# Optimization experiments

Hardware: AMD Instinct MI355X
Metric: run time of the kernel (lower is better)

## Reference

```python
import jax, jax.numpy as jnp
import numpy as np

DIM = 1024
HEADS = 16


def setup_inputs() -> dict:
    key = jax.random.key(0)
    ks = jax.random.split(key, 5)
    x = jax.random.normal(ks[0], (2, 2048, DIM), dtype=jnp.float32)
    # nn.Linear init-like scaling
    qkv_w = jax.random.normal(ks[1], (3 * DIM, DIM), dtype=jnp.float32) * (1.0 / np.sqrt(DIM))
    qkv_b = jax.random.normal(ks[2], (3 * DIM,), dtype=jnp.float32) * 0.02
    proj_w = jax.random.normal(ks[3], (DIM, DIM), dtype=jnp.float32) * (1.0 / np.sqrt(DIM))
    proj_b = jax.random.normal(ks[4], (DIM,), dtype=jnp.float32) * 0.02
    return {"x": x, "qkv_w": qkv_w, "qkv_b": qkv_b, "proj_w": proj_w, "proj_b": proj_b}


def reference(x, qkv_w, qkv_b, proj_w, proj_b):
    B, N, C = x.shape
    H = HEADS
    Dh = C // H
    scale = Dh ** -0.5
    # qkv: [B, N, 3C] -> [3, B, H, N, Dh]
    qkv = (x @ qkv_w.T + qkv_b).reshape(B, N, 3, H, Dh).transpose(2, 0, 3, 1, 4)
    q, k, v = qkv[0], qkv[1], qkv[2]
    attn = jnp.einsum('bhnd,bhmd->bhnm', q, k) * scale
    attn = jax.nn.softmax(attn, axis=-1)
    out = jnp.einsum('bhnm,bhmd->bhnd', attn, v)  # [B, H, N, Dh]
    out = out.transpose(0, 2, 1, 3).reshape(B, N, C)
    return out @ proj_w.T + proj_b
```

## Files before the change

kernel.cpp:

```cpp
#include <hip/hip_runtime.h>
#include <stdint.h>

#define DIM    1024
#define NHEADS 16
#define DH     64
#define SEQ    2048
#define BATCH  2
#define BHEADS (BATCH * NHEADS)
#define MROWS  (BATCH * SEQ)
#define SL2E   0.18033688011112042f

typedef __attribute__((ext_vector_type(8))) short bf16x8;
typedef __attribute__((ext_vector_type(4))) float f32x4;
typedef unsigned short ushort_t;

#define GLDS(gp, lp) __builtin_amdgcn_global_load_lds( \
    (__attribute__((address_space(1))) void*)(gp), \
    (__attribute__((address_space(3))) void*)(lp), 16, 0, 0)

__device__ inline ushort_t f2bf(float f) {
    unsigned u = __builtin_bit_cast(unsigned, f);
    u += 0x7FFFu + ((u >> 16) & 1u);
    return (ushort_t)(u >> 16);
}

__global__ __launch_bounds__(256) void cvt_kernel(
    const float* __restrict__ s0, const float* __restrict__ s1, const float* __restrict__ s2,
    ushort_t* __restrict__ d0, ushort_t* __restrict__ d1, ushort_t* __restrict__ d2)
{
    const int N0 = MROWS * DIM;
    const int N1 = 3 * DIM * DIM;
    const int N2 = DIM * DIM;
    int e = (blockIdx.x * 256 + threadIdx.x) << 2;
    const float* src; ushort_t* dst;
    if (e < N0)                { src = s0 + e;             dst = d0 + e; }
    else if (e < N0 + N1)      { src = s1 + (e - N0);      dst = d1 + (e - N0); }
    else if (e < N0 + N1 + N2) { src = s2 + (e - N0 - N1); dst = d2 + (e - N0 - N1); }
    else return;
    float4 f = *(const float4*)src;
    ushort4 o;
    o.x = f2bf(f.x); o.y = f2bf(f.y); o.z = f2bf(f.z); o.w = f2bf(f.w);
    *(ushort4*)dst = o;
}

__global__ __launch_bounds__(256) void qkv_gemm(
    const ushort_t* __restrict__ A, const ushort_t* __restrict__ W,
    const float* __restrict__ bias,
    ushort_t* __restrict__ Qw, ushort_t* __restrict__ Kw, ushort_t* __restrict__ Vt)
{
    __shared__ ushort_t smem[128 * 136];
    ushort_t* As = smem;
    ushort_t* Bs = smem + 128 * 64;

    const int tid  = threadIdx.x;
    const int lane = tid & 63;
    const int wave = tid >> 6;
    const int quad = lane >> 4;
    const int l16  = lane & 15;
    const int wm   = (wave >> 1) * 64;
    const int wn   = (wave & 1) * 64;
    const int bm   = blockIdx.x * 128;
    const int bn   = blockIdx.y * 128;
    const int Rl   = lane >> 3;
    const int pp   = lane & 7;

    f32x4 acc[4][4];
    for (int i = 0; i < 4; i++)
        for (int j = 0; j < 4; j++)
            for (int r = 0; r < 4; r++) acc[i][j][r] = 0.f;

    for (int kk = 0; kk < DIM; kk += 64) {
        __syncthreads();
        for (int j = 0; j < 4; j++) {
            int Rb = j * 32 + wave * 8;
            int R  = Rb + Rl;
            int c  = pp ^ (R & 7);
            GLDS(A + (size_t)(bm + R) * DIM + kk + c * 8, As + Rb * 64 + lane * 8);
            GLDS(W + (size_t)(bn + R) * DIM + kk + c * 8, Bs + Rb * 64 + lane * 8);
        }
        __syncthreads();

        for (int kh = 0; kh < 2; kh++) {
            bf16x8 a[4], b[4];
            for (int mi = 0; mi < 4; mi++) {
                int r = wm + mi * 16 + l16;
                a[mi] = *(const bf16x8*)(As + r * 64 + (((kh * 4 + quad) ^ (r & 7)) << 3));
            }
            for (int ni = 0; ni < 4; ni++) {
                int r = wn + ni * 16 + l16;
                b[ni] = *(const bf16x8*)(Bs + r * 64 + (((kh * 4 + quad) ^ (r & 7)) << 3));
            }
            for (int mi = 0; mi < 4; mi++)
                for (int ni = 0; ni < 4; ni++)
                    acc[mi][ni] = __builtin_amdgcn_mfma_f32_16x16x32_bf16(a[mi], b[ni], acc[mi][ni], 0, 0, 0);
        }
    }

    __syncthreads();
    const int three = bn >> 10;
    const float scale = (three == 0) ? SL2E : 1.0f;
    for (int ni = 0; ni < 4; ni++) {
        int cl   = wn + ni * 16 + l16;
        float bv = bias[bn + cl];
        for (int mi = 0; mi < 4; mi++)
            for (int reg = 0; reg < 4; reg++) {
                int r = wm + mi * 16 + quad * 4 + reg;
                smem[r * 136 + cl] = f2bf((acc[mi][ni][reg] + bv) * scale);
            }
    }
    __syncthreads();

    const int b = bm >> 11, npos0 = bm & 2047;
    if (three < 2) {
        int r = tid >> 1, hh = tid & 1;
        int hc = (bn + hh * 64) & 1023;
        int h  = hc >> 6;
        ushort_t* dst = (three == 0 ? Qw : Kw) + ((size_t)(b * NHEADS + h) * SEQ + npos0 + r) * DH;
        const ushort_t* srcp = smem + r * 136 + hh * 64;
        for (int s = 0; s < 8; s++)
            *(uint4*)(dst + s * 8) = *(const uint4*)(srcp + s * 8);
    } else {
        int c = tid & 127, hh = tid >> 7;
        int hc = (bn + c) & 1023;
        int h  = hc >> 6, d = hc & 63;
        ushort_t* dst = Vt + ((size_t)(b * NHEADS + h) * DH + d) * SEQ + npos0 + hh * 64;
        for (int s = 0; s < 8; s++) {
            union { ushort_t u[8]; uint4 v; } tmp;
            for (int k2 = 0; k2 < 8; k2++)
                tmp.u[k2] = smem[(hh * 64 + s * 8 + k2) * 136 + c];
            *(uint4*)(dst + s * 8) = tmp.v;
        }
    }
}

struct AttnSmem {
    ushort_t KV[2][2][2][32 * 64];
    ushort_t QP[128 * 64];
};
union AttnSmemU {
    AttnSmem m;
    float Lb[128][66];
};

__global__ __launch_bounds__(512, 4) void attn_kernel(
    const ushort_t* __restrict__ Qw, const ushort_t* __restrict__ Kw,
    const ushort_t* __restrict__ Vt, ushort_t* __restrict__ Ao)
{
    __shared__ AttnSmemU sh;

    const int tid  = threadIdx.x;
    const int lane = tid & 63;
    const int wave = tid >> 6;
    const int grp  = wave >> 2;
    const int wg   = wave & 3;
    const int quad = lane >> 4;
    const int l16  = lane & 15;
    const int bh   = blockIdx.y;
    const int q0   = blockIdx.x * 128;
    const int Rl   = lane >> 3;
    const int pp   = lane & 7;

    const ushort_t* Qh = Qw + (size_t)bh * SEQ * DH;
    const ushort_t* Kh = Kw + (size_t)bh * SEQ * DH;
    const ushort_t* Vh = Vt + (size_t)bh * DH * SEQ;

    for (int j = 0; j < 2; j++) {
        int Rb = j * 64 + wave * 8;
        int R  = Rb + Rl;
        int c  = pp ^ (R & 7);
        GLDS(Qh + (size_t)(q0 + R) * DH + c * 8, sh.m.QP + Rb * 64 + lane * 8);
    }
    {
        int t  = grp;
        int Rk = wg * 8 + Rl;
        int ck = pp ^ (Rk & 7);
        GLDS(Kh + (size_t)(t * 32 + Rk) * DH + ck * 8, sh.m.KV[0][grp][0] + wg * 512 + lane * 8);
        int Rv = wg * 16 + (lane >> 2);
        int pv = lane & 3;
        int cv = pv ^ ((Rv >> 1) & 3);
        GLDS(Vh + (size_t)Rv * SEQ + t * 32 + cv * 8, sh.m.KV[0][grp][1] + wg * 512 + lane * 8);
    }
    __syncthreads();

    bf16x8 qf[2][2];
    for (int mi = 0; mi < 2; mi++)
        for (int kh = 0; kh < 2; kh++) {
            int r = wg * 32 + mi * 16 + l16;
            qf[mi][kh] = *(const bf16x8*)(sh.m.QP + r * 64 + (((kh * 4 + quad) ^ (r & 7)) << 3));
        }
    __syncthreads();

    bf16x8 vones;
    for (int i = 0; i < 8; i++) vones[i] = (short)0x3F80;

    f32x4 oacc[2][4], liacc[2];
    for (int mi = 0; mi < 2; mi++) {
        for (int r = 0; r < 4; r++) liacc[mi][r] = 0.f;
        for (int d = 0; d < 4; d++)
            for (int r = 0; r < 4; r++) oacc[mi][d][r] = 0.f;
    }

    ushort_t* Pw = sh.m.QP + wave * 1024;

    const int NIT = 32;
    for (int it = 0; it < NIT; it++) {
        const int phase = it & 1;
        if (it < NIT - 1) {
            int np = phase ^ 1;
            int t  = 2 * (it + 1) + grp;
            int Rk = wg * 8 + Rl;
            int ck = pp ^ (Rk & 7);
            GLDS(Kh + (size_t)(t * 32 + Rk) * DH + ck * 8, sh.m.KV[np][grp][0] + wg * 512 + lane * 8);
            int Rv = wg * 16 + (lane >> 2);
            int pv = lane & 3;
            int cv = pv ^ ((Rv >> 1) & 3);
            GLDS(Vh + (size_t)Rv * SEQ + t * 32 + cv * 8, sh.m.KV[np][grp][1] + wg * 512 + lane * 8);
        }
        const ushort_t* Ksb = sh.m.KV[phase][grp][0];
        const ushort_t* Vsb = sh.m.KV[phase][grp][1];

        f32x4 s[2][2];
        for (int mi = 0; mi < 2; mi++)
            for (int nf = 0; nf < 2; nf++)
                for (int r = 0; r < 4; r++) s[mi][nf][r] = 0.f;
        for (int kh = 0; kh < 2; kh++)
            for (int nf = 0; nf < 2; nf++) {
                int r = nf * 16 + l16;
                bf16x8 kf = *(const bf16x8*)(Ksb + r * 64 + (((kh * 4 + quad) ^ (r & 7)) << 3));
                s[0][nf] = __builtin_amdgcn_mfma_f32_16x16x32_bf16(kf, qf[0][kh], s[0][nf], 0, 0, 0);
                s[1][nf] = __builtin_amdgcn_mfma_f32_16x16x32_bf16(kf, qf[1][kh], s[1][nf], 0, 0, 0);
            }

        for (int mi = 0; mi < 2; mi++) {
            int row = mi * 16 + l16;
            int swz = (row >> 1) & 3;
            for (int nf = 0; nf < 2; nf++) {
                unsigned u0 = __builtin_bit_cast(unsigned, __builtin_amdgcn_exp2f(s[mi][nf][0])) + 0x8000u;
                unsigned u1 = __builtin_bit_cast(unsigned, __builtin_amdgcn_exp2f(s[mi][nf][1])) + 0x8000u;
                unsigned u2 = __builtin_bit_cast(unsigned, __builtin_amdgcn_exp2f(s[mi][nf][2])) + 0x8000u;
                unsigned u3 = __builtin_bit_cast(unsigned, __builtin_amdgcn_exp2f(s[mi][nf][3])) + 0x8000u;
                uint2 pk;
                pk.x = __builtin_amdgcn_perm(u1, u0, 0x07060302u);
                pk.y = __builtin_amdgcn_perm(u3, u2, 0x07060302u);
                int jp = (nf * 2 + (quad >> 1)) ^ swz;
                *(uint2*)(Pw + row * 32 + jp * 8 + (quad & 1) * 4) = pk;
            }
        }

        bf16x8 pf[2];
        for (int mi = 0; mi < 2; mi++) {
            int row = mi * 16 + l16;
            int jp  = quad ^ ((row >> 1) & 3);
            pf[mi] = *(const bf16x8*)(Pw + row * 32 + jp * 8);
        }

        liacc[0] = __builtin_amdgcn_mfma_f32_16x16x32_bf16(pf[0], vones, liacc[0], 0, 0, 0);
        liacc[1] = __builtin_amdgcn_mfma_f32_16x16x32_bf16(pf[1], vones, liacc[1], 0, 0, 0);

        for (int df = 0; df < 4; df++) {
            int r  = df * 16 + l16;
            int jp = quad ^ ((r >> 1) & 3);
            bf16x8 vf = *(const bf16x8*)(Vsb + r * 32 + jp * 8);
            oacc[0][df] = __builtin_amdgcn_mfma_f32_16x16x32_bf16(pf[0], vf, oacc[0][df], 0, 0, 0);
            oacc[1][df] = __builtin_amdgcn_mfma_f32_16x16x32_bf16(pf[1], vf, oacc[1][df], 0, 0, 0);
        }

        __syncthreads();
    }

    const int b = bh >> 4, h = bh & 15;
    if (grp == 1) {
        for (int mi = 0; mi < 2; mi++)
            for (int reg = 0; reg < 4; reg++) {
                int row = wg * 32 + mi * 16 + quad * 4 + reg;
                for (int df = 0; df < 4; df++)
                    sh.Lb[row][df * 16 + l16] = oacc[mi][df][reg];
                if (l16 == 0) sh.Lb[row][64] = liacc[mi][reg];
            }
    }
    __syncthreads();
    if (grp == 0) {
        for (int mi = 0; mi < 2; mi++)
            for (int reg = 0; reg < 4; reg++) {
                int row   = wg * 32 + mi * 16 + quad * 4 + reg;
                float inv = 1.0f / (liacc[mi][reg] + sh.Lb[row][64]);
                int grow  = q0 + row;
                for (int df = 0; df < 4; df++) {
                    int col = df * 16 + l16;
                    float o = oacc[mi][df][reg] + sh.Lb[row][col];
                    Ao[((size_t)b * SEQ + grow) * DIM + h * 64 + col] = f2bf(o * inv);
                }
            }
    }
}

__global__ __launch_bounds__(256, 4) void proj_gemm(
    const ushort_t* __restrict__ A, const ushort_t* __restrict__ W,
    const float* __restrict__ bias, float* __restrict__ Cout)
{
    __shared__ ushort_t As[128 * 64];
    __shared__ ushort_t Bs[64 * 64];

    const int tid  = threadIdx.x;
    const int lane = tid & 63;
    const int wave = tid >> 6;
    const int quad = lane >> 4;
    const int l16  = lane & 15;
    const int wm   = (wave >> 1) * 64;
    const int wn   = (wave & 1) * 32;
    const int bm   = blockIdx.x * 128;
    const int bn   = blockIdx.y * 64;
    const int Rl   = lane >> 3;
    const int pp   = lane & 7;

    f32x4 acc[4][2];
    for (int i = 0; i < 4; i++)
        for (int j = 0; j < 2; j++)
            for (int r = 0; r < 4; r++) acc[i][j][r] = 0.f;

    for (int kk = 0; kk < DIM; kk += 64) {
        __syncthreads();
        for (int j = 0; j < 4; j++) {
            int Rb = j * 32 + wave * 8;
            int R  = Rb + Rl;
            int c  = pp ^ (R & 7);
            GLDS(A + (size_t)(bm + R) * DIM + kk + c * 8, As + Rb * 64 + lane * 8);
        }
        for (int j = 0; j < 2; j++) {
            int Rb = j * 32 + wave * 8;
            int R  = Rb + Rl;
            int c  = pp ^ (R & 7);
            GLDS(W + (size_t)(bn + R) * DIM + kk + c * 8, Bs + Rb * 64 + lane * 8);
        }
        __syncthreads();

        for (int kh = 0; kh < 2; kh++) {
            bf16x8 a[4], b[2];
            for (int mi = 0; mi < 4; mi++) {
                int r = wm + mi * 16 + l16;
                a[mi] = *(const bf16x8*)(As + r * 64 + (((kh * 4 + quad) ^ (r & 7)) << 3));
            }
            for (int ni = 0; ni < 2; ni++) {
                int r = wn + ni * 16 + l16;
                b[ni] = *(const bf16x8*)(Bs + r * 64 + (((kh * 4 + quad) ^ (r & 7)) << 3));
            }
            for (int mi = 0; mi < 4; mi++)
                for (int ni = 0; ni < 2; ni++)
                    acc[mi][ni] = __builtin_amdgcn_mfma_f32_16x16x32_bf16(a[mi], b[ni], acc[mi][ni], 0, 0, 0);
        }
    }

    for (int mi = 0; mi < 4; mi++) {
        for (int ni = 0; ni < 2; ni++) {
            int col  = bn + wn + ni * 16 + l16;
            float bv = bias[col];
            for (int reg = 0; reg < 4; reg++) {
                int row = bm + wm + mi * 16 + quad * 4 + reg;
                Cout[(size_t)row * DIM + col] = acc[mi][ni][reg] + bv;
            }
        }
    }
}

extern "C" void kernel_launch(void* const* d_in, const int* in_sizes, int n_in,
                              void* d_out, int out_size, void* d_ws, size_t ws_size,
                              hipStream_t stream) {
    const float* x      = (const float*)d_in[0];
    const float* qkv_w  = (const float*)d_in[1];
    const float* qkv_b  = (const float*)d_in[2];
    const float* proj_w = (const float*)d_in[3];
    const float* proj_b = (const float*)d_in[4];
    float* out = (float*)d_out;

    ushort_t* xb      = (ushort_t*)d_ws;
    ushort_t* qkv_wb  = xb      + (size_t)MROWS * DIM;
    ushort_t* proj_wb = qkv_wb  + (size_t)3 * DIM * DIM;
    ushort_t* Qw      = proj_wb + (size_t)DIM * DIM;
    ushort_t* Kw      = Qw      + (size_t)BHEADS * SEQ * DH;
    ushort_t* Vt      = Kw      + (size_t)BHEADS * SEQ * DH;
    ushort_t* Ao      = Vt      + (size_t)BHEADS * SEQ * DH;

    const int total_cvt = MROWS * DIM + 3 * DIM * DIM + DIM * DIM;
    cvt_kernel<<<total_cvt / (4 * 256), 256, 0, stream>>>(x, qkv_w, proj_w, xb, qkv_wb, proj_wb);
    qkv_gemm<<<dim3(MROWS / 128, (3 * DIM) / 128), 256, 0, stream>>>(xb, qkv_wb, qkv_b, Qw, Kw, Vt);
    attn_kernel<<<dim3(SEQ / 128, BHEADS), 512, 0, stream>>>(Qw, Kw, Vt, Ao);
    proj_gemm<<<dim3(MROWS / 128, DIM / 64), 256, 0, stream>>>(Ao, proj_wb, proj_b, out);
}
```

Baseline: 190.5 us.

## Double-buffer LDS tiles in QKV and projection GEMMs to overlap loads

Both GEMM kernels now keep two LDS stages and issue the global-to-LDS loads for the next K tile before computing on the current one. Explicit vmcnt waits and raw barriers replace the two __syncthreads per iteration. The goal is to hide global memory latency behind MFMA work. In exchange, shared memory use per block roughly doubles, which can lower occupancy, and the hand-counted vmcnt values must match the number of loads in flight.

```diff
diff --git a/kernel.cpp b/kernel.cpp
--- a/kernel.cpp
+++ b/kernel.cpp
@@ -48,9 +48,10 @@
     const float* __restrict__ bias,
     ushort_t* __restrict__ Qw, ushort_t* __restrict__ Kw, ushort_t* __restrict__ Vt)
 {
-    __shared__ ushort_t smem[128 * 136];
-    ushort_t* As = smem;
-    ushort_t* Bs = smem + 128 * 64;
+    __shared__ union {
+        ushort_t stage[2][2][128 * 64];
+        ushort_t T[128 * 136];
+    } sm;
 
     const int tid  = threadIdx.x;
     const int lane = tid & 63;
@@ -69,34 +70,53 @@
         for (int j = 0; j < 4; j++)
             for (int r = 0; r < 4; r++) acc[i][j][r] = 0.f;
 
-    for (int kk = 0; kk < DIM; kk += 64) {
-        __syncthreads();
-        for (int j = 0; j < 4; j++) {
-            int Rb = j * 32 + wave * 8;
-            int R  = Rb + Rl;
-            int c  = pp ^ (R & 7);
-            GLDS(A + (size_t)(bm + R) * DIM + kk + c * 8, As + Rb * 64 + lane * 8);
-            GLDS(W + (size_t)(bn + R) * DIM + kk + c * 8, Bs + Rb * 64 + lane * 8);
-        }
-        __syncthreads();
-
+    for (int j = 0; j < 4; j++) {
+        int Rb = j * 32 + wave * 8;
+        int R  = Rb + Rl;
+        int c  = pp ^ (R & 7);
+        GLDS(A + (size_t)(bm + R) * DIM + c * 8, sm.stage[0][0] + Rb * 64 + lane * 8);
+        GLDS(W + (size_t)(bn + R) * DIM + c * 8, sm.stage[0][1] + Rb * 64 + lane * 8);
+    }
+
+    const int NT = DIM / 64;
+    for (int t = 0; t < NT; t++) {
+        if (t < NT - 1) {
+            int kk = (t + 1) * 64;
+            ushort_t* As1 = sm.stage[(t + 1) & 1][0];
+            ushort_t* Bs1 = sm.stage[(t + 1) & 1][1];
+            for (int j = 0; j < 4; j++) {
+                int Rb = j * 32 + wave * 8;
+                int R  = Rb + Rl;
+                int c  = pp ^ (R & 7);
+                GLDS(A + (size_t)(bm + R) * DIM + kk + c * 8, As1 + Rb * 64 + lane * 8);
+                GLDS(W + (size_t)(bn + R) * DIM + kk + c * 8, Bs1 + Rb * 64 + lane * 8);
+            }
+            __asm volatile("s_waitcnt vmcnt(8)" ::: "memory");
+        } else {
+            __asm volatile("s_waitcnt vmcnt(0)" ::: "memory");
+        }
+        __asm volatile("s_barrier" ::: "memory");
+
+        const ushort_t* Asb = sm.stage[t & 1][0];
+        const ushort_t* Bsb = sm.stage[t & 1][1];
         for (int kh = 0; kh < 2; kh++) {
             bf16x8 a[4], b[4];
             for (int mi = 0; mi < 4; mi++) {
                 int r = wm + mi * 16 + l16;
-                a[mi] = *(const bf16x8*)(As + r * 64 + (((kh * 4 + quad) ^ (r & 7)) << 3));
+                a[mi] = *(const bf16x8*)(Asb + r * 64 + (((kh * 4 + quad) ^ (r & 7)) << 3));
             }
             for (int ni = 0; ni < 4; ni++) {
                 int r = wn + ni * 16 + l16;
-                b[ni] = *(const bf16x8*)(Bs + r * 64 + (((kh * 4 + quad) ^ (r & 7)) << 3));
+                b[ni] = *(const bf16x8*)(Bsb + r * 64 + (((kh * 4 + quad) ^ (r & 7)) << 3));
             }
             for (int mi = 0; mi < 4; mi++)
                 for (int ni = 0; ni < 4; ni++)
                     acc[mi][ni] = __builtin_amdgcn_mfma_f32_16x16x32_bf16(a[mi], b[ni], acc[mi][ni], 0, 0, 0);
         }
-    }
-
-    __syncthreads();
+        __asm volatile("s_waitcnt lgkmcnt(0)" ::: "memory");
+        __asm volatile("s_barrier" ::: "memory");
+    }
+
     const int three = bn >> 10;
     const float scale = (three == 0) ? SL2E : 1.0f;
     for (int ni = 0; ni < 4; ni++) {
@@ -105,7 +125,7 @@
         for (int mi = 0; mi < 4; mi++)
             for (int reg = 0; reg < 4; reg++) {
                 int r = wm + mi * 16 + quad * 4 + reg;
-                smem[r * 136 + cl] = f2bf((acc[mi][ni][reg] + bv) * scale);
+                sm.T[r * 136 + cl] = f2bf((acc[mi][ni][reg] + bv) * scale);
             }
     }
     __syncthreads();
@@ -116,7 +136,7 @@
         int hc = (bn + hh * 64) & 1023;
         int h  = hc >> 6;
         ushort_t* dst = (three == 0 ? Qw : Kw) + ((size_t)(b * NHEADS + h) * SEQ + npos0 + r) * DH;
-        const ushort_t* srcp = smem + r * 136 + hh * 64;
+        const ushort_t* srcp = sm.T + r * 136 + hh * 64;
         for (int s = 0; s < 8; s++)
             *(uint4*)(dst + s * 8) = *(const uint4*)(srcp + s * 8);
     } else {
@@ -127,7 +147,7 @@
         for (int s = 0; s < 8; s++) {
             union { ushort_t u[8]; uint4 v; } tmp;
             for (int k2 = 0; k2 < 8; k2++)
-                tmp.u[k2] = smem[(hh * 64 + s * 8 + k2) * 136 + c];
+                tmp.u[k2] = sm.T[(hh * 64 + s * 8 + k2) * 136 + c];
             *(uint4*)(dst + s * 8) = tmp.v;
         }
     }
@@ -298,8 +318,8 @@
     const ushort_t* __restrict__ A, const ushort_t* __restrict__ W,
     const float* __restrict__ bias, float* __restrict__ Cout)
 {
-    __shared__ ushort_t As[128 * 64];
-    __shared__ ushort_t Bs[64 * 64];
+    __shared__ ushort_t Asd[2][128 * 64];
+    __shared__ ushort_t Bsd[2][64 * 64];
 
     const int tid  = threadIdx.x;
     const int lane = tid & 63;
@@ -318,36 +338,61 @@
         for (int j = 0; j < 2; j++)
             for (int r = 0; r < 4; r++) acc[i][j][r] = 0.f;
 
-    for (int kk = 0; kk < DIM; kk += 64) {
-        __syncthreads();
-        for (int j = 0; j < 4; j++) {
-            int Rb = j * 32 + wave * 8;
-            int R  = Rb + Rl;
-            int c  = pp ^ (R & 7);
-            GLDS(A + (size_t)(bm + R) * DIM + kk + c * 8, As + Rb * 64 + lane * 8);
-        }
-        for (int j = 0; j < 2; j++) {
-            int Rb = j * 32 + wave * 8;
-            int R  = Rb + Rl;
-            int c  = pp ^ (R & 7);
-            GLDS(W + (size_t)(bn + R) * DIM + kk + c * 8, Bs + Rb * 64 + lane * 8);
-        }
-        __syncthreads();
-
+    for (int j = 0; j < 4; j++) {
+        int Rb = j * 32 + wave * 8;
+        int R  = Rb + Rl;
+        int c  = pp ^ (R & 7);
+        GLDS(A + (size_t)(bm + R) * DIM + c * 8, Asd[0] + Rb * 64 + lane * 8);
+    }
+    for (int j = 0; j < 2; j++) {
+        int Rb = j * 32 + wave * 8;
+        int R  = Rb + Rl;
+        int c  = pp ^ (R & 7);
+        GLDS(W + (size_t)(bn + R) * DIM + c * 8, Bsd[0] + Rb * 64 + lane * 8);
+    }
+
+    const int NT = DIM / 64;
+    for (int t = 0; t < NT; t++) {
+        if (t < NT - 1) {
+            int kk = (t + 1) * 64;
+            ushort_t* As1 = Asd[(t + 1) & 1];
+            ushort_t* Bs1 = Bsd[(t + 1) & 1];
+            for (int j = 0; j < 4; j++) {
+                int Rb = j * 32 + wave * 8;
+                int R  = Rb + Rl;
+                int c  = pp ^ (R & 7);
+                GLDS(A + (size_t)(bm + R) * DIM + kk + c * 8, As1 + Rb * 64 + lane * 8);
+            }
+            for (int j = 0; j < 2; j++) {
+                int Rb = j * 32 + wave * 8;
+                int R  = Rb + Rl;
+                int c  = pp ^ (R & 7);
+                GLDS(W + (size_t)(bn + R) * DIM + kk + c * 8, Bs1 + Rb * 64 + lane * 8);
+            }
+            __asm volatile("s_waitcnt vmcnt(6)" ::: "memory");
+        } else {
+            __asm volatile("s_waitcnt vmcnt(0)" ::: "memory");
+        }
+        __asm volatile("s_barrier" ::: "memory");
+
+        const ushort_t* Asb = Asd[t & 1];
+        const ushort_t* Bsb = Bsd[t & 1];
         for (int kh = 0; kh < 2; kh++) {
             bf16x8 a[4], b[2];
             for (int mi = 0; mi < 4; mi++) {
                 int r = wm + mi * 16 + l16;
-                a[mi] = *(const bf16x8*)(As + r * 64 + (((kh * 4 + quad) ^ (r & 7)) << 3));
+                a[mi] = *(const bf16x8*)(Asb + r * 64 + (((kh * 4 + quad) ^ (r & 7)) << 3));
             }
             for (int ni = 0; ni < 2; ni++) {
                 int r = wn + ni * 16 + l16;
-                b[ni] = *(const bf16x8*)(Bs + r * 64 + (((kh * 4 + quad) ^ (r & 7)) << 3));
+                b[ni] = *(const bf16x8*)(Bsb + r * 64 + (((kh * 4 + quad) ^ (r & 7)) << 3));
             }
             for (int mi = 0; mi < 4; mi++)
                 for (int ni = 0; ni < 2; ni++)
                     acc[mi][ni] = __builtin_amdgcn_mfma_f32_16x16x32_bf16(a[mi], b[ni], acc[mi][ni], 0, 0, 0);
         }
+        __asm volatile("s_waitcnt lgkmcnt(0)" ::: "memory");
+        __asm volatile("s_barrier" ::: "memory");
     }
 
     for (int mi = 0; mi < 4; mi++) {
```

After: 182.5 us. -4.2%, faster.
